# Kernel optimization log

Measured on AMD Instinct MI355X. Metric: run time of the kernel, lower is better.

Reference implementation:

```python
import jax, jax.numpy as jnp
import numpy as np

B, K, D = 8, 2048, 1024

def setup_inputs() -> dict:
    key = jax.random.key(0)
    k1, k2 = jax.random.split(key)
    x = jax.random.normal(k1, (B, K, D), dtype=jnp.float32)
    W = jax.random.normal(k2, (K, K), dtype=jnp.float32) * 0.02  # dt_proj weight [out=K, in=K]
    b = jnp.zeros((K,), dtype=jnp.float32)                        # dt_proj bias
    return {"x": x, "W": W, "b": b}

def _scan_combine(c1, c2):
    # compose affine maps s -> a*s + u; (a1,u1) then (a2,u2)
    a1, u1 = c1
    a2, u2 = c2
    return (a2 * a1, a2 * u1 + u2)

def reference(x, W, b):
    # lam[b,t,d] = sigmoid( sum_k x[b,k,d] * W[t,k] + b[t] )
    # (dt_proj is a Linear over the TIME axis after permute(0,2,1))
    lam = jax.nn.sigmoid(jnp.einsum('bkd,tk->btd', x, W) + b[None, :, None])
    # s_t = lam_t * s_{t-1} + (1 - lam_t) * x_t, s_0 = 0  -> associative scan over time
    _, ys = jax.lax.associative_scan(_scan_combine, (lam, (1.0 - lam) * x), axis=1)
    return ys
```

## Files before the change

kernel.cpp:

```cpp
#include <hip/hip_runtime.h>
#include <hip/hip_bf16.h>
#include <stdint.h>

#define B_ 8
#define K_ 2048
#define D_ 1024
#define NC 32
#define TC (K_ / NC)

typedef float v4f __attribute__((ext_vector_type(4)));
typedef short v8s __attribute__((ext_vector_type(8)));

__device__ __forceinline__ unsigned short f2bf(float f) {
    __hip_bfloat16 h = __float2bfloat16(f);
    return *reinterpret_cast<unsigned short*>(&h);
}

__device__ __forceinline__ void async_ld16(const void* g, void* l) {
    __builtin_amdgcn_global_load_lds(
        (__attribute__((address_space(1))) void*)(void*)g,
        (__attribute__((address_space(3))) void*)l,
        16, 0, 0);
}

__global__ void conv_w(const float* __restrict__ W, unsigned short* __restrict__ Wb) {
    int i = (blockIdx.x * 256 + threadIdx.x) * 4;
    float4 v = *(const float4*)(W + i);
    ushort4 o;
    o.x = f2bf(v.x); o.y = f2bf(v.y); o.z = f2bf(v.z); o.w = f2bf(v.w);
    *(ushort4*)(Wb + i) = o;
}

__global__ void conv_x_t(const float* __restrict__ x, unsigned short* __restrict__ xT) {
    const int k0 = blockIdx.x * 64, d0 = blockIdx.y * 64, bb = blockIdx.z;
    __shared__ unsigned short tile[64][68];
    const int tid = threadIdx.x;
    const int tx = tid & 15, ty = tid >> 4;
    const float* xp = x + (size_t)bb * K_ * D_;
#pragma unroll
    for (int r = 0; r < 4; r++) {
        int row = ty + r * 16;
        float4 v = *(const float4*)(xp + (size_t)(k0 + row) * D_ + d0 + tx * 4);
        tile[row][tx * 4 + 0] = f2bf(v.x);
        tile[row][tx * 4 + 1] = f2bf(v.y);
        tile[row][tx * 4 + 2] = f2bf(v.z);
        tile[row][tx * 4 + 3] = f2bf(v.w);
    }
    __syncthreads();
    unsigned short* op = xT + (size_t)bb * D_ * K_;
#pragma unroll
    for (int r = 0; r < 4; r++) {
        int dcol = ty + r * 16;
        ushort4 u;
        u.x = tile[tx * 4 + 0][dcol];
        u.y = tile[tx * 4 + 1][dcol];
        u.z = tile[tx * 4 + 2][dcol];
        u.w = tile[tx * 4 + 3][dcol];
        *(ushort4*)(op + (size_t)(d0 + dcol) * K_ + k0 + tx * 4) = u;
    }
}

__launch_bounds__(256)
__global__ void gemm_sig(const unsigned short* __restrict__ Wb,
                         const unsigned short* __restrict__ xT,
                         const float* __restrict__ bias,
                         float* __restrict__ lam) {
    const int tM = blockIdx.x, tN = blockIdx.y, bb = blockIdx.z;
    __shared__ unsigned short As[2][128 * 32];
    __shared__ unsigned short Bs[2][128 * 32];
    const int tid = threadIdx.x;
    const int w = tid >> 6;
    const int lane = tid & 63;
    const int wm = w >> 1, wn = w & 1;
    const int quad = lane >> 4;
    const int l16 = lane & 15;

    v4f acc[4][4];
#pragma unroll
    for (int i = 0; i < 4; i++)
#pragma unroll
        for (int j = 0; j < 4; j++) acc[i][j] = (v4f)0.f;

    const unsigned short* Ag = Wb + (size_t)(tM * 128) * K_;
    const unsigned short* Bg = xT + (size_t)bb * D_ * K_ + (size_t)(tN * 128) * K_;

    const int srow = lane >> 2;
    const int schunk = (lane & 3) * 8;

    for (int k0 = 0; k0 < K_; k0 += 64) {
#pragma unroll
        for (int h = 0; h < 2; h++) {
#pragma unroll
            for (int q = 0; q < 2; q++) {
                int rb = (q * 4 + w) * 16;
                async_ld16(Ag + (size_t)(rb + srow) * K_ + k0 + h * 32 + schunk, &As[h][rb * 32]);
                async_ld16(Bg + (size_t)(rb + srow) * K_ + k0 + h * 32 + schunk, &Bs[h][rb * 32]);
            }
        }
        __syncthreads();
#pragma unroll
        for (int h = 0; h < 2; h++) {
            v8s af[4], bfr[4];
#pragma unroll
            for (int i = 0; i < 4; i++)
                af[i] = *(const v8s*)(&As[h][(wm * 64 + i * 16 + l16) * 32 + quad * 8]);
#pragma unroll
            for (int j = 0; j < 4; j++)
                bfr[j] = *(const v8s*)(&Bs[h][(wn * 64 + j * 16 + l16) * 32 + quad * 8]);
#pragma unroll
            for (int i = 0; i < 4; i++)
#pragma unroll
                for (int j = 0; j < 4; j++)
                    acc[i][j] = __builtin_amdgcn_mfma_f32_16x16x32_bf16(af[i], bfr[j], acc[i][j], 0, 0, 0);
        }
        __syncthreads();
    }

    float* out = lam + (size_t)bb * K_ * D_;
#pragma unroll
    for (int i = 0; i < 4; i++) {
        int rowb = tM * 128 + wm * 64 + i * 16 + quad * 4;
#pragma unroll
        for (int r = 0; r < 4; r++) {
            float bt = bias[rowb + r];
#pragma unroll
            for (int j = 0; j < 4; j++) {
                int col = tN * 128 + wn * 64 + j * 16 + l16;
                float v = acc[i][j][r] + bt;
                out[(size_t)(rowb + r) * D_ + col] = 1.f / (1.f + __expf(-v));
            }
        }
    }
}

__global__ void scan_pass1(const float* __restrict__ lam, const float* __restrict__ x,
                           float* __restrict__ Ac, float* __restrict__ Uc) {
    int id = blockIdx.x * 256 + threadIdx.x;
    int d2 = (id & 511) * 2;
    int c = (id >> 9) & (NC - 1);
    int bb = id >> 14;
    const float* lp = lam + ((size_t)bb * K_ + (size_t)c * TC) * D_ + d2;
    const float* xp = x   + ((size_t)bb * K_ + (size_t)c * TC) * D_ + d2;
    float2 A = make_float2(1.f, 1.f), U = make_float2(0.f, 0.f);
#pragma unroll 8
    for (int t = 0; t < TC; t++) {
        float2 l  = *(const float2*)(lp + (size_t)t * D_);
        float2 xv = *(const float2*)(xp + (size_t)t * D_);
        A.x *= l.x; A.y *= l.y;
        U.x = l.x * U.x + (1.f - l.x) * xv.x;
        U.y = l.y * U.y + (1.f - l.y) * xv.y;
    }
    size_t oi = ((size_t)bb * NC + c) * D_ + d2;
    *(float2*)(Ac + oi) = A;
    *(float2*)(Uc + oi) = U;
}

__global__ void scan_pass2(const float* __restrict__ Ac, const float* __restrict__ Uc,
                           float* __restrict__ Sin) {
    int id = blockIdx.x * 256 + threadIdx.x;
    int d = id & (D_ - 1);
    int bb = id >> 10;
    float s = 0.f;
#pragma unroll
    for (int c = 0; c < NC; c++) {
        int idx = (bb * NC + c) * D_ + d;
        Sin[idx] = s;
        s = Ac[idx] * s + Uc[idx];
    }
}

__global__ void scan_pass3(const float* __restrict__ x, const float* __restrict__ Sin,
                           float* __restrict__ lamout) {
    int id = blockIdx.x * 256 + threadIdx.x;
    int d2 = (id & 511) * 2;
    int c = (id >> 9) & (NC - 1);
    int bb = id >> 14;
    float* lp = lamout + ((size_t)bb * K_ + (size_t)c * TC) * D_ + d2;
    const float* xp = x + ((size_t)bb * K_ + (size_t)c * TC) * D_ + d2;
    size_t si = ((size_t)bb * NC + c) * D_ + d2;
    float2 s = *(const float2*)(Sin + si);
#pragma unroll 8
    for (int t = 0; t < TC; t++) {
        float2 l  = *(const float2*)(lp + (size_t)t * D_);
        float2 xv = *(const float2*)(xp + (size_t)t * D_);
        s.x = l.x * s.x + (1.f - l.x) * xv.x;
        s.y = l.y * s.y + (1.f - l.y) * xv.y;
        *(float2*)(lp + (size_t)t * D_) = s;
    }
}

extern "C" void kernel_launch(void* const* d_in, const int* in_sizes, int n_in,
                              void* d_out, int out_size, void* d_ws, size_t ws_size,
                              hipStream_t stream) {
    const float* x    = (const float*)d_in[0];
    const float* W    = (const float*)d_in[1];
    const float* bias = (const float*)d_in[2];
    float* out = (float*)d_out;
    char* ws = (char*)d_ws;

    unsigned short* xT = (unsigned short*)ws;
    unsigned short* Wb = (unsigned short*)(ws + 33554432);
    float* Ac  = (float*)(ws + 33554432);
    float* Uc  = (float*)(ws + 33554432 + 1048576);
    float* Sin = (float*)(ws + 33554432 + 2097152);

    conv_w<<<dim3(K_ * K_ / 4 / 256), 256, 0, stream>>>(W, Wb);
    conv_x_t<<<dim3(K_ / 64, D_ / 64, B_), 256, 0, stream>>>(x, xT);
    gemm_sig<<<dim3(K_ / 128, D_ / 128, B_), 256, 0, stream>>>(Wb, xT, bias, out);
    scan_pass1<<<dim3(B_ * NC * D_ / 2 / 256), 256, 0, stream>>>(out, x, Ac, Uc);
    scan_pass2<<<dim3(B_ * D_ / 256), 256, 0, stream>>>(Ac, Uc, Sin);
    scan_pass3<<<dim3(B_ * NC * D_ / 2 / 256), 256, 0, stream>>>(x, Sin, out);
}
```

Baseline: 275.7 us.

## Restructure GEMM into 256x256 tiles with double-buffered async loads and swizzled LDS

Rewrites the bf16 MFMA GEMM to use 256x256 output tiles with 512 threads and a 1D grid remapped for XCD locality. Global-to-LDS loads go into a double buffer and are interleaved with MFMA phases using explicit waitcnt, barriers and setprio. LDS rows are XOR-swizzled to reduce bank conflicts. The aim is more data reuse per block and overlap of memory with compute. The cost is higher register pressure from 32 accumulators and only 256 blocks, which may underfill the device.

```diff
diff --git a/kernel.cpp b/kernel.cpp
--- a/kernel.cpp
+++ b/kernel.cpp
@@ -60,72 +60,140 @@
     }
 }
 
-__launch_bounds__(256)
+__launch_bounds__(512, 2)
 __global__ void gemm_sig(const unsigned short* __restrict__ Wb,
                          const unsigned short* __restrict__ xT,
                          const float* __restrict__ bias,
                          float* __restrict__ lam) {
-    const int tM = blockIdx.x, tN = blockIdx.y, bb = blockIdx.z;
-    __shared__ unsigned short As[2][128 * 32];
-    __shared__ unsigned short Bs[2][128 * 32];
+    __shared__ unsigned short As[2][2][256 * 32];
+    __shared__ unsigned short Bs[2][2][256 * 32];
+
+    const int bid = blockIdx.x;
+    const int lid = (bid & 7) * 32 + (bid >> 3);
+    const int bb = lid >> 5;
+    const int tM = (lid >> 2) & 7;
+    const int tN = lid & 3;
+
     const int tid = threadIdx.x;
     const int w = tid >> 6;
     const int lane = tid & 63;
-    const int wm = w >> 1, wn = w & 1;
+    const int wm = w >> 2;
+    const int wn = w & 3;
     const int quad = lane >> 4;
     const int l16 = lane & 15;
 
-    v4f acc[4][4];
-#pragma unroll
-    for (int i = 0; i < 4; i++)
+    const unsigned short* Ag = Wb + (size_t)(tM * 256) * K_;
+    const unsigned short* Bg = xT + (size_t)bb * D_ * K_ + (size_t)(tN * 256) * K_;
+
+    const int srow = lane >> 2;
+    const int sgk8 = ((lane & 3) ^ ((lane >> 3) & 3)) * 8;
+
+    const int frg = (quad ^ ((l16 >> 1) & 3)) * 8;
+    const int aoff = (wm * 128 + l16) * 32 + frg;
+    const int boff = (wn * 64 + l16) * 32 + frg;
+
+    v4f acc[8][4];
+#pragma unroll
+    for (int i = 0; i < 8; i++)
 #pragma unroll
         for (int j = 0; j < 4; j++) acc[i][j] = (v4f)0.f;
 
-    const unsigned short* Ag = Wb + (size_t)(tM * 128) * K_;
-    const unsigned short* Bg = xT + (size_t)bb * D_ * K_ + (size_t)(tN * 128) * K_;
-
-    const int srow = lane >> 2;
-    const int schunk = (lane & 3) * 8;
-
-    for (int k0 = 0; k0 < K_; k0 += 64) {
-#pragma unroll
-        for (int h = 0; h < 2; h++) {
-#pragma unroll
-            for (int q = 0; q < 2; q++) {
-                int rb = (q * 4 + w) * 16;
-                async_ld16(Ag + (size_t)(rb + srow) * K_ + k0 + h * 32 + schunk, &As[h][rb * 32]);
-                async_ld16(Bg + (size_t)(rb + srow) * K_ + k0 + h * 32 + schunk, &Bs[h][rb * 32]);
-            }
-        }
-        __syncthreads();
-#pragma unroll
-        for (int h = 0; h < 2; h++) {
-            v8s af[4], bfr[4];
-#pragma unroll
-            for (int i = 0; i < 4; i++)
-                af[i] = *(const v8s*)(&As[h][(wm * 64 + i * 16 + l16) * 32 + quad * 8]);
-#pragma unroll
-            for (int j = 0; j < 4; j++)
-                bfr[j] = *(const v8s*)(&Bs[h][(wn * 64 + j * 16 + l16) * 32 + quad * 8]);
-#pragma unroll
-            for (int i = 0; i < 4; i++)
-#pragma unroll
-                for (int j = 0; j < 4; j++)
-                    acc[i][j] = __builtin_amdgcn_mfma_f32_16x16x32_bf16(af[i], bfr[j], acc[i][j], 0, 0, 0);
-        }
-        __syncthreads();
-    }
+#define STAGE_(dst, bufi, kh, kk, Gp)                                                   \
+    do {                                                                                \
+        async_ld16(Gp + (size_t)(w * 16 + srow) * K_ + (kk) + (kh) * 32 + sgk8,         \
+                   &dst[bufi][kh][w * 512]);                                            \
+        async_ld16(Gp + (size_t)((8 + w) * 16 + srow) * K_ + (kk) + (kh) * 32 + sgk8,   \
+                   &dst[bufi][kh][(8 + w) * 512]);                                      \
+    } while (0)
+
+    STAGE_(As, 0, 0, 0, Ag);
+    STAGE_(Bs, 0, 0, 0, Bg);
+    STAGE_(As, 0, 1, 0, Ag);
+    STAGE_(Bs, 0, 1, 0, Bg);
+    asm volatile("s_waitcnt vmcnt(4)");
+    asm volatile("s_barrier" ::: "memory");
+
+    v8s af[8], bf[2];
+
+    for (int t = 0; t < K_ / 64; ++t) {
+        const int cur = t & 1, nxt = cur ^ 1;
+        int k1 = (t + 1) * 64;
+        if (k1 == K_) k1 = 0;
+
+#pragma unroll
+        for (int i = 0; i < 8; i++) af[i] = *(const v8s*)(&As[cur][0][aoff + i * 512]);
+        bf[0] = *(const v8s*)(&Bs[cur][0][boff]);
+        bf[1] = *(const v8s*)(&Bs[cur][0][boff + 512]);
+        STAGE_(As, nxt, 0, k1, Ag);
+        asm volatile("s_barrier" ::: "memory");
+        asm volatile("s_waitcnt lgkmcnt(0)");
+        __builtin_amdgcn_s_setprio(1);
+#pragma unroll
+        for (int i = 0; i < 8; i++) {
+            acc[i][0] = __builtin_amdgcn_mfma_f32_16x16x32_bf16(af[i], bf[0], acc[i][0], 0, 0, 0);
+            acc[i][1] = __builtin_amdgcn_mfma_f32_16x16x32_bf16(af[i], bf[1], acc[i][1], 0, 0, 0);
+        }
+        __builtin_amdgcn_s_setprio(0);
+        asm volatile("s_barrier" ::: "memory");
+
+        bf[0] = *(const v8s*)(&Bs[cur][0][boff + 2 * 512]);
+        bf[1] = *(const v8s*)(&Bs[cur][0][boff + 3 * 512]);
+        STAGE_(Bs, nxt, 0, k1, Bg);
+        asm volatile("s_barrier" ::: "memory");
+        asm volatile("s_waitcnt lgkmcnt(0)");
+        __builtin_amdgcn_s_setprio(1);
+#pragma unroll
+        for (int i = 0; i < 8; i++) {
+            acc[i][2] = __builtin_amdgcn_mfma_f32_16x16x32_bf16(af[i], bf[0], acc[i][2], 0, 0, 0);
+            acc[i][3] = __builtin_amdgcn_mfma_f32_16x16x32_bf16(af[i], bf[1], acc[i][3], 0, 0, 0);
+        }
+        __builtin_amdgcn_s_setprio(0);
+        asm volatile("s_waitcnt vmcnt(4)");
+        asm volatile("s_barrier" ::: "memory");
+
+#pragma unroll
+        for (int i = 0; i < 8; i++) af[i] = *(const v8s*)(&As[cur][1][aoff + i * 512]);
+        bf[0] = *(const v8s*)(&Bs[cur][1][boff]);
+        bf[1] = *(const v8s*)(&Bs[cur][1][boff + 512]);
+        STAGE_(As, nxt, 1, k1, Ag);
+        asm volatile("s_barrier" ::: "memory");
+        asm volatile("s_waitcnt lgkmcnt(0)");
+        __builtin_amdgcn_s_setprio(1);
+#pragma unroll
+        for (int i = 0; i < 8; i++) {
+            acc[i][0] = __builtin_amdgcn_mfma_f32_16x16x32_bf16(af[i], bf[0], acc[i][0], 0, 0, 0);
+            acc[i][1] = __builtin_amdgcn_mfma_f32_16x16x32_bf16(af[i], bf[1], acc[i][1], 0, 0, 0);
+        }
+        __builtin_amdgcn_s_setprio(0);
+        asm volatile("s_barrier" ::: "memory");
+
+        bf[0] = *(const v8s*)(&Bs[cur][1][boff + 2 * 512]);
+        bf[1] = *(const v8s*)(&Bs[cur][1][boff + 3 * 512]);
+        STAGE_(Bs, nxt, 1, k1, Bg);
+        asm volatile("s_barrier" ::: "memory");
+        asm volatile("s_waitcnt lgkmcnt(0)");
+        __builtin_amdgcn_s_setprio(1);
+#pragma unroll
+        for (int i = 0; i < 8; i++) {
+            acc[i][2] = __builtin_amdgcn_mfma_f32_16x16x32_bf16(af[i], bf[0], acc[i][2], 0, 0, 0);
+            acc[i][3] = __builtin_amdgcn_mfma_f32_16x16x32_bf16(af[i], bf[1], acc[i][3], 0, 0, 0);
+        }
+        __builtin_amdgcn_s_setprio(0);
+        asm volatile("s_waitcnt vmcnt(4)");
+        asm volatile("s_barrier" ::: "memory");
+    }
+#undef STAGE_
 
     float* out = lam + (size_t)bb * K_ * D_;
 #pragma unroll
-    for (int i = 0; i < 4; i++) {
-        int rowb = tM * 128 + wm * 64 + i * 16 + quad * 4;
+    for (int i = 0; i < 8; i++) {
+        int rowb = tM * 256 + wm * 128 + i * 16 + quad * 4;
 #pragma unroll
         for (int r = 0; r < 4; r++) {
             float bt = bias[rowb + r];
 #pragma unroll
             for (int j = 0; j < 4; j++) {
-                int col = tN * 128 + wn * 64 + j * 16 + l16;
+                int col = tN * 256 + wn * 64 + j * 16 + l16;
                 float v = acc[i][j][r] + bt;
                 out[(size_t)(rowb + r) * D_ + col] = 1.f / (1.f + __expf(-v));
             }
@@ -206,7 +274,7 @@
 
     conv_w<<<dim3(K_ * K_ / 4 / 256), 256, 0, stream>>>(W, Wb);
     conv_x_t<<<dim3(K_ / 64, D_ / 64, B_), 256, 0, stream>>>(x, xT);
-    gemm_sig<<<dim3(K_ / 128, D_ / 128, B_), 256, 0, stream>>>(Wb, xT, bias, out);
+    gemm_sig<<<dim3(256), dim3(512), 0, stream>>>(Wb, xT, bias, out);
     scan_pass1<<<dim3(B_ * NC * D_ / 2 / 256), 256, 0, stream>>>(out, x, Ac, Uc);
     scan_pass2<<<dim3(B_ * D_ / 256), 256, 0, stream>>>(Ac, Uc, Sin);
     scan_pass3<<<dim3(B_ * NC * D_ / 2 / 256), 256, 0, stream>>>(x, Sin, out);
```

Measured after the change: 244.2 us. -11.4%, faster.
